# Kernel tuning notes

Measured on AMD Instinct MI355X. Metric: run time of the kernel, lower is better.

The kernel has to match this reference:

```python
import jax, jax.numpy as jnp
import numpy as np

B, H, W = 512, 36, 36
N = H * W          # 1296 oscillators
K = 8              # couplings per oscillator
EP0 = 0.1          # kura_update_rate
ANNEAL = 0.5


def setup_inputs() -> dict:
    key = jax.random.key(0)
    k = jax.random.split(key, 8)
    return {
        "input": jax.random.normal(k[0], (B, H, W), jnp.float32),
        "initial_phase": jax.random.uniform(k[1], (B, N), jnp.float32) * (2.0 * np.pi),
        "connectivity": jax.random.randint(k[2], (B, N, K), 0, N),
        "episodes": 25,
        "conv1_w": jax.random.normal(k[3], (8, 1, 3, 3), jnp.float32) * 0.1,
        "conv1_b": jnp.zeros((8,), jnp.float32),
        "conv2_w": jax.random.normal(k[4], (16, 8, 3, 3), jnp.float32) * 0.1,
        "conv2_b": jnp.zeros((16,), jnp.float32),
        "conv3_w": jax.random.normal(k[5], (32, 16, 3, 3), jnp.float32) * 0.1,
        "conv3_b": jnp.zeros((32,), jnp.float32),
        "fc_w": jax.random.normal(k[6], (108 * 8, 108 * 32), jnp.float32) * 0.02,
        "fc_b": jnp.zeros((108 * 8,), jnp.float32),
    }


def _conv3x3(x, w, b):
    y = jax.lax.conv_general_dilated(
        x, w, (1, 1), "SAME", dimension_numbers=("NCHW", "OIHW", "NCHW"))
    return y + b[None, :, None, None]


def _kuramoto(initial_phase, coupling, connectivity, steps, ep0):
    # phase: [B,N]; coupling: [B,N,K]; connectivity: [B,N,K] neighbor indices
    gather = jax.vmap(lambda p, c: p[c])  # -> [B,N,K] neighbor phases

    def step(carry, i):
        phase, ep = carry
        neigh = gather(phase, connectivity)
        # d(phase_i) = ep * sum_j coupling_ij * sin(phase_j - phase_i)
        delta = ep * (coupling * jnp.sin(neigh - phase[:, :, None])).sum(-1)
        phase = phase + delta
        ep = ep - ANNEAL * i * ep / steps  # annealed update rate
        return (phase, ep), phase

    (_, _), phases = jax.lax.scan(
        step, (initial_phase, jnp.float32(ep0)),
        jnp.arange(steps, dtype=jnp.float32))
    # record=True: trajectory includes the initial phase
    return jnp.concatenate([initial_phase[None], phases], axis=0)  # [steps+1,B,N]


def reference(input, initial_phase, connectivity, episodes,
              conv1_w, conv1_b, conv2_w, conv2_b, conv3_w, conv3_b, fc_w, fc_b):
    x = input.reshape(-1, 1, 36, 36)
    c1 = jax.nn.relu(_conv3x3(x, conv1_w, conv1_b))
    c2 = jax.nn.relu(_conv3x3(c1, conv2_w, conv2_b))
    c3 = jax.nn.sigmoid(_conv3x3(c2, conv3_w, conv3_b))
    fc = (c3.reshape(-1, 108 * 32) @ fc_w.T + fc_b).reshape(-1, N, K)  # [B,1296,8]
    phase_list = _kuramoto(initial_phase, fc, connectivity, episodes, EP0)
    return phase_list, fc
```

## Files before the change

kernel.cpp:

```cpp
#include <hip/hip_runtime.h>
#include <hip/hip_bf16.h>

#define NPOS 1296
#define BATCH 512
#define STEPS 25
#define PH_STRIDE (BATCH * NPOS)
#define PH_TOTAL ((STEPS + 1) * PH_STRIDE)
#define FC_K 3456
#define FC_N 864
#define FC_NPAD 896
#define FC_M 6144
#define KT_ITERS 54

typedef float f32x4 __attribute__((ext_vector_type(4)));
typedef __bf16 bf16x8 __attribute__((ext_vector_type(8)));

__device__ __forceinline__ ushort f2bf(float f) {
  union { float f; unsigned u; } v; v.f = f;
  unsigned r = v.u + 0x7FFFu + ((v.u >> 16) & 1u);
  return (ushort)(r >> 16);
}
__device__ __forceinline__ float bf2f(ushort h) {
  union { unsigned u; float f; } v; v.u = ((unsigned)h) << 16; return v.f;
}

__device__ __forceinline__ void async_copy16(void* lds, const void* g) {
  __builtin_amdgcn_global_load_lds(
      (const __attribute__((address_space(1))) unsigned*)g,
      (__attribute__((address_space(3))) unsigned*)lds, 16, 0, 0);
}
__device__ __forceinline__ void raw_barrier() { asm volatile("s_barrier" ::: "memory"); }
__device__ __forceinline__ void waitcnt_vm7() { asm volatile("s_waitcnt vmcnt(7)" ::: "memory"); }
__device__ __forceinline__ void waitcnt_vm0() { asm volatile("s_waitcnt vmcnt(0)" ::: "memory"); }

__global__ __launch_bounds__(256) void wprep_kernel(
    const float* __restrict__ w1, const float* __restrict__ w2, const float* __restrict__ w3,
    float* __restrict__ w1t, ushort* __restrict__ w2t, ushort* __restrict__ w3t) {
  const int tid = threadIdx.x;
  for (int i = tid; i < 72; i += 256) {
    const int s = i / 8, co = i - s * 8;
    w1t[i] = w1[co * 9 + s];
  }
  for (int i = tid; i < 16 * 96; i += 256) {
    const int co = i / 96, k = i - co * 96;
    const int s = k / 8, ci = k - s * 8;
    w2t[i] = (k < 72) ? f2bf(w2[(co * 8 + ci) * 9 + s]) : (ushort)0;
  }
  for (int i = tid; i < 32 * 160; i += 256) {
    const int co = i / 160, k = i - co * 160;
    const int s = k / 16, ci = k - s * 16;
    w3t[i] = (k < 144) ? f2bf(w3[(co * 16 + ci) * 9 + s]) : (ushort)0;
  }
}

__global__ __launch_bounds__(256, 4) void conv_fused_kernel(
    const float* __restrict__ in, const float* __restrict__ w1t, const float* __restrict__ b1,
    const ushort* __restrict__ w2t, const float* __restrict__ b2,
    const ushort* __restrict__ w3t, const float* __restrict__ b3,
    ushort* __restrict__ aout) {
  __shared__ __align__(16) float sIn[18][40];
  __shared__ __align__(16) ushort sC1[18][40][8];
  __shared__ __align__(16) ushort sC2[16][40][16];
  const int b = blockIdx.x, band = blockIdx.y, tid = threadIdx.x;
  const int r0 = band * 12;
  const int wave = tid >> 6, lane = tid & 63;
  const int quad = lane >> 4, l16 = lane & 15;
  {
    const uint4 zz = make_uint4(0, 0, 0, 0);
    for (int i = tid; i < 180; i += 256) ((uint4*)sIn)[i] = zz;
    for (int i = tid; i < 720; i += 256) ((uint4*)sC1)[i] = zz;
    for (int i = tid; i < 1280; i += 256) ((uint4*)sC2)[i] = zz;
  }
  __syncthreads();
  for (int i = tid; i < 18 * 18; i += 256) {
    const int r = i / 18, c = i - r * 18;
    const int gy = r0 - 3 + r;
    if ((unsigned)gy < 36u)
      *(float2*)&sIn[r][2 + 2 * c] = *(const float2*)(in + (size_t)b * NPOS + gy * 36 + 2 * c);
  }
  __syncthreads();
  for (int i = tid; i < 16 * 36; i += 256) {
    const int lr = i / 36, x = i - lr * 36;
    float acc[8];
#pragma unroll
    for (int co = 0; co < 8; ++co) acc[co] = b1[co];
#pragma unroll
    for (int s = 0; s < 9; ++s) {
      const int dy = s / 3, dx = s - 3 * dy;
      const float v = sIn[lr + dy][x + 1 + dx];
#pragma unroll
      for (int co = 0; co < 8; ++co) acc[co] = fmaf(w1t[s * 8 + co], v, acc[co]);
    }
    const int g1 = r0 - 2 + lr;
    if ((unsigned)g1 < 36u) {
      uint4 pk;
      pk.x = (uint)f2bf(fmaxf(acc[0], 0.f)) | ((uint)f2bf(fmaxf(acc[1], 0.f)) << 16);
      pk.y = (uint)f2bf(fmaxf(acc[2], 0.f)) | ((uint)f2bf(fmaxf(acc[3], 0.f)) << 16);
      pk.z = (uint)f2bf(fmaxf(acc[4], 0.f)) | ((uint)f2bf(fmaxf(acc[5], 0.f)) << 16);
      pk.w = (uint)f2bf(fmaxf(acc[6], 0.f)) | ((uint)f2bf(fmaxf(acc[7], 0.f)) << 16);
      *(uint4*)&sC1[lr][x + 2][0] = pk;
    }
  }
  __syncthreads();
  bf16x8 w2f[3];
#pragma unroll
  for (int f = 0; f < 3; ++f)
    w2f[f] = *(const bf16x8*)(w2t + l16 * 96 + f * 32 + quad * 8);
  const float bias2 = b2[l16];
  for (int chunk = wave; chunk < 32; chunk += 4) {
    const int m = chunk * 16 + l16;
    const int oy = m / 36, x = m - oy * 36;
    f32x4 acc = {0.f, 0.f, 0.f, 0.f};
#pragma unroll
    for (int f = 0; f < 3; ++f) {
      const int s0 = 4 * f + quad;
      const int dy = s0 / 3, dx = s0 - 3 * dy;
      const bf16x8 af = *(const bf16x8*)&sC1[oy + dy][x + 1 + dx][0];
      acc = __builtin_amdgcn_mfma_f32_16x16x32_bf16(af, w2f[f], acc, 0, 0, 0);
    }
#pragma unroll
    for (int r = 0; r < 4; ++r) {
      const int px = chunk * 16 + quad * 4 + r;
      const int oy2 = px / 36, x2 = px - oy2 * 36;
      const int g2 = r0 - 1 + oy2;
      if (px < 504 && (unsigned)g2 < 36u)
        sC2[oy2][x2 + 2][l16] = f2bf(fmaxf(acc[r] + bias2, 0.f));
    }
  }
  __syncthreads();
  bf16x8 w3f[2][5];
#pragma unroll
  for (int t = 0; t < 2; ++t)
#pragma unroll
    for (int f = 0; f < 5; ++f)
      w3f[t][f] = *(const bf16x8*)(w3t + (t * 16 + l16) * 160 + f * 32 + quad * 8);
  const float bias3a = b3[l16], bias3b = b3[16 + l16];
  ushort* ob = aout + (size_t)b * (32 * NPOS) + r0 * 36;
  for (int chunk = wave; chunk < 27; chunk += 4) {
    const int m = chunk * 16 + l16;
    const int oy = m / 36, x = m - oy * 36;
    f32x4 acc0 = {0.f, 0.f, 0.f, 0.f}, acc1 = {0.f, 0.f, 0.f, 0.f};
#pragma unroll
    for (int f = 0; f < 5; ++f) {
      const int s0 = 2 * f + (quad >> 1);
      const int dy = s0 / 3, dx = s0 - 3 * dy;
      const bf16x8 af = *(const bf16x8*)&sC2[oy + dy][x + 1 + dx][(quad & 1) * 8];
      acc0 = __builtin_amdgcn_mfma_f32_16x16x32_bf16(af, w3f[0][f], acc0, 0, 0, 0);
      acc1 = __builtin_amdgcn_mfma_f32_16x16x32_bf16(af, w3f[1][f], acc1, 0, 0, 0);
    }
    const int pxb = chunk * 16 + quad * 4;
    ushort4 pk;
#pragma unroll
    for (int r = 0; r < 4; ++r)
      ((ushort*)&pk)[r] = f2bf(1.f / (1.f + __expf(-(acc0[r] + bias3a))));
    *(ushort4*)(ob + (size_t)l16 * NPOS + pxb) = pk;
#pragma unroll
    for (int r = 0; r < 4; ++r)
      ((ushort*)&pk)[r] = f2bf(1.f / (1.f + __expf(-(acc1[r] + bias3b))));
    *(ushort4*)(ob + (size_t)(16 + l16) * NPOS + pxb) = pk;
  }
}

__global__ __launch_bounds__(256) void wcvt_kernel(const float* __restrict__ w, ushort* __restrict__ wb) {
  const int idx = blockIdx.x * 256 + threadIdx.x;
  if (idx >= FC_NPAD * FC_K) return;
  const int n = idx / FC_K;
  wb[idx] = (n < FC_N) ? f2bf(w[idx]) : (ushort)0;
}

__global__ __launch_bounds__(256) void gemm_kernel(
    const ushort* __restrict__ A, const ushort* __restrict__ Bt,
    const float* __restrict__ bias, float* __restrict__ C) {
  __shared__ __align__(16) ushort smem[2][14336];
  const int tid = threadIdx.x;
  const int lin = blockIdx.x;
  const int xcd = lin & 7, g = lin >> 3;
  const int bn = g % 7;
  const int bm = xcd + 8 * (g / 7);
  const int row0 = bm * 96, col0 = bn * 128;
  const int wave = tid >> 6, lane = tid & 63;
  const int wr = (wave >> 1) * 48, wc = (wave & 1) * 64;
  const int quad = lane >> 4, l16 = lane & 15;
  const int oswz = (quad ^ ((l16 >> 1) & 3)) * 8;
  f32x4 acc[3][4] = {};

  const int rr = lane >> 2;
  const int soct = ((lane & 3) ^ ((lane >> 3) & 3)) * 8;
  const ushort* gsrc[7];
  const ushort* ldst[7];
  {
    const int s = wave >> 1;
    if ((wave & 1) == 0) {
#pragma unroll
      for (int j = 0; j < 6; ++j) {
        gsrc[j] = A + ((size_t)row0 + j * 16 + rr) * FC_K + s * 32 + soct;
        ldst[j] = &smem[0][s * 3072 + j * 512];
      }
      gsrc[6] = Bt + ((size_t)col0 + rr) * FC_K + s * 32 + soct;
      ldst[6] = &smem[0][6144 + s * 4096];
    } else {
#pragma unroll
      for (int j = 0; j < 7; ++j) {
        gsrc[j] = Bt + ((size_t)col0 + (j + 1) * 16 + rr) * FC_K + s * 32 + soct;
        ldst[j] = &smem[0][6144 + s * 4096 + (j + 1) * 512];
      }
    }
  }
#pragma unroll
  for (int j = 0; j < 7; ++j) async_copy16((void*)ldst[j], gsrc[j]);
#pragma unroll
  for (int j = 0; j < 7; ++j) async_copy16((void*)(ldst[j] + 14336), gsrc[j] + 64);

  for (int kt = 0; kt < KT_ITERS; ++kt) {
    const int p = kt & 1;
    waitcnt_vm7();
    raw_barrier();
    const ushort* base = &smem[p][0];
#pragma unroll
    for (int s = 0; s < 2; ++s) {
      bf16x8 af[3], bfr[4];
#pragma unroll
      for (int t = 0; t < 3; ++t)
        af[t] = *(const bf16x8*)(base + s * 3072 + (wr + t * 16 + l16) * 32 + oswz);
#pragma unroll
      for (int t = 0; t < 4; ++t)
        bfr[t] = *(const bf16x8*)(base + 6144 + s * 4096 + (wc + t * 16 + l16) * 32 + oswz);
#pragma unroll
      for (int tm = 0; tm < 3; ++tm)
#pragma unroll
        for (int tn = 0; tn < 4; ++tn)
          acc[tm][tn] = __builtin_amdgcn_mfma_f32_16x16x32_bf16(af[tm], bfr[tn], acc[tm][tn], 0, 0, 0);
    }
    raw_barrier();
    int kn = kt + 2;
    if (kn >= KT_ITERS) kn -= KT_ITERS;
    const int koff = kn * 64;
#pragma unroll
    for (int j = 0; j < 7; ++j) async_copy16((void*)(ldst[j] + p * 14336), gsrc[j] + koff);
  }
  waitcnt_vm0();

#pragma unroll
  for (int tn = 0; tn < 4; ++tn) {
    const int col = col0 + wc + tn * 16 + l16;
    if (col < FC_N) {
      const float bv = bias[col];
#pragma unroll
      for (int tm = 0; tm < 3; ++tm) {
#pragma unroll
        for (int r = 0; r < 4; ++r) {
          const int row = row0 + wr + tm * 16 + quad * 4 + r;
          C[(size_t)row * FC_N + col] = acc[tm][tn][r] + bv;
        }
      }
    }
  }
}

__global__ __launch_bounds__(512) void kuramoto_kernel(
    const float* __restrict__ ph0, const int* __restrict__ conn,
    const float* __restrict__ cpl, float* __restrict__ out) {
  __shared__ float2 sc[2][NPOS];
  const int b = blockIdx.x, tid = threadIdx.x;
  int rj[3][8];
  float rc[3][8];
  float myph[3];
  float2 mysc[3];
#pragma unroll
  for (int s = 0; s < 3; ++s) {
    const int i = tid + s * 512;
    if (i < NPOS) {
      const float p = ph0[(size_t)b * NPOS + i];
      myph[s] = p;
      __builtin_nontemporal_store(p, out + (size_t)b * NPOS + i);
      float sn, cn;
      __sincosf(p, &sn, &cn);
      mysc[s] = make_float2(sn, cn);
      sc[0][i] = mysc[s];
      const size_t base = (size_t)b * (NPOS * 8) + (size_t)i * 8;
      const int4 j0 = *(const int4*)(conn + base);
      const int4 j1 = *(const int4*)(conn + base + 4);
      const float4 c0 = *(const float4*)(cpl + base);
      const float4 c1 = *(const float4*)(cpl + base + 4);
      rj[s][0] = j0.x; rj[s][1] = j0.y; rj[s][2] = j0.z; rj[s][3] = j0.w;
      rj[s][4] = j1.x; rj[s][5] = j1.y; rj[s][6] = j1.z; rj[s][7] = j1.w;
      rc[s][0] = c0.x; rc[s][1] = c0.y; rc[s][2] = c0.z; rc[s][3] = c0.w;
      rc[s][4] = c1.x; rc[s][5] = c1.y; rc[s][6] = c1.z; rc[s][7] = c1.w;
    }
  }
  float ep = 0.1f;
  for (int t = 0; t < STEPS; ++t) {
    __syncthreads();
    const int cur = t & 1;
    float* op = out + (size_t)(t + 1) * PH_STRIDE + (size_t)b * NPOS;
#pragma unroll
    for (int s = 0; s < 3; ++s) {
      const int i = tid + s * 512;
      if (i < NPOS) {
        float ss = 0.f, cc = 0.f;
#pragma unroll
        for (int k = 0; k < 8; ++k) {
          const float2 v = sc[cur][rj[s][k]];
          ss = fmaf(rc[s][k], v.x, ss);
          cc = fmaf(rc[s][k], v.y, cc);
        }
        const float np = myph[s] + ep * (mysc[s].y * ss - mysc[s].x * cc);
        myph[s] = np;
        __builtin_nontemporal_store(np, op + i);
        float sn, cn;
        __sincosf(np, &sn, &cn);
        mysc[s] = make_float2(sn, cn);
        sc[cur ^ 1][i] = mysc[s];
      }
    }
    ep = ep * (1.0f - 0.02f * (float)t);
  }
}

extern "C" void kernel_launch(void* const* d_in, const int* in_sizes, int n_in,
                              void* d_out, int out_size, void* d_ws, size_t ws_size,
                              hipStream_t stream) {
  const float* input = (const float*)d_in[0];
  const float* ph0   = (const float*)d_in[1];
  const int*   conn  = (const int*)d_in[2];
  const float* w1 = (const float*)d_in[4];
  const float* b1 = (const float*)d_in[5];
  const float* w2 = (const float*)d_in[6];
  const float* b2 = (const float*)d_in[7];
  const float* w3 = (const float*)d_in[8];
  const float* b3 = (const float*)d_in[9];
  const float* fcw = (const float*)d_in[10];
  const float* fcb = (const float*)d_in[11];
  float* out = (float*)d_out;

  ushort* Abuf = (ushort*)d_ws;
  ushort* Wbuf = (ushort*)((char*)d_ws + 42467328);
  float*  w1t  = (float*)((char*)d_ws + 48660480);
  ushort* w2t  = (ushort*)((char*)d_ws + 48660768);
  ushort* w3t  = (ushort*)((char*)d_ws + 48663840);
  float* fcout = out + PH_TOTAL;

  wprep_kernel<<<1, 256, 0, stream>>>(w1, w2, w3, w1t, w2t, w3t);
  wcvt_kernel<<<(FC_NPAD * FC_K) / 256, 256, 0, stream>>>(fcw, Wbuf);
  conv_fused_kernel<<<dim3(BATCH, 3), 256, 0, stream>>>(input, w1t, b1, w2t, b2, w3t, b3, Abuf);
  gemm_kernel<<<448, 256, 0, stream>>>(Abuf, Wbuf, fcb, fcout);
  kuramoto_kernel<<<BATCH, 512, 0, stream>>>(ph0, conn, fcout, out);
}
```

Baseline: 249.1 us.

## Fuse conv, FC GEMM and Kuramoto into one persistent megakernel with grid barriers

Replaces the five separate launches (weight prep, weight conversion, conv, GEMM, Kuramoto) with a single persistent kernel of 512 blocks. Phases are separated by atomic grid barriers, and a memset resets the barrier counters on each call. This removes launch gaps and inter-kernel drain. Small conv weights are now transposed into LDS per block, and the Kuramoto stage runs 256 threads per batch with 6 oscillators per thread instead of 512 threads. The costs are higher register pressure, a launch-bounds occupancy target of 2 blocks per CU, lower parallelism in the Kuramoto stage, and reliance on all 512 blocks being co-resident for the barriers to avoid deadlock.

```diff
diff --git a/kernel.cpp b/kernel.cpp
--- a/kernel.cpp
+++ b/kernel.cpp
@@ -9,8 +9,9 @@
 #define FC_K 3456
 #define FC_N 864
 #define FC_NPAD 896
-#define FC_M 6144
 #define KT_ITERS 54
+#define NBLK 512
+#define NTHR 256
 
 typedef float f32x4 __attribute__((ext_vector_type(4)));
 typedef __bf16 bf16x8 __attribute__((ext_vector_type(8)));
@@ -20,9 +21,6 @@
   unsigned r = v.u + 0x7FFFu + ((v.u >> 16) & 1u);
   return (ushort)(r >> 16);
 }
-__device__ __forceinline__ float bf2f(ushort h) {
-  union { unsigned u; float f; } v; v.u = ((unsigned)h) << 16; return v.f;
-}
 
 __device__ __forceinline__ void async_copy16(void* lds, const void* g) {
   __builtin_amdgcn_global_load_lds(
@@ -33,287 +31,304 @@
 __device__ __forceinline__ void waitcnt_vm7() { asm volatile("s_waitcnt vmcnt(7)" ::: "memory"); }
 __device__ __forceinline__ void waitcnt_vm0() { asm volatile("s_waitcnt vmcnt(0)" ::: "memory"); }
 
-__global__ __launch_bounds__(256) void wprep_kernel(
-    const float* __restrict__ w1, const float* __restrict__ w2, const float* __restrict__ w3,
-    float* __restrict__ w1t, ushort* __restrict__ w2t, ushort* __restrict__ w3t) {
-  const int tid = threadIdx.x;
-  for (int i = tid; i < 72; i += 256) {
-    const int s = i / 8, co = i - s * 8;
-    w1t[i] = w1[co * 9 + s];
+__device__ __forceinline__ void grid_barrier(int* bar) {
+  __threadfence();
+  __syncthreads();
+  if (threadIdx.x == 0) {
+    __hip_atomic_fetch_add(bar, 1, __ATOMIC_RELEASE, __HIP_MEMORY_SCOPE_AGENT);
+    while (__hip_atomic_load(bar, __ATOMIC_ACQUIRE, __HIP_MEMORY_SCOPE_AGENT) < NBLK)
+      __builtin_amdgcn_s_sleep(2);
   }
-  for (int i = tid; i < 16 * 96; i += 256) {
-    const int co = i / 96, k = i - co * 96;
-    const int s = k / 8, ci = k - s * 8;
-    w2t[i] = (k < 72) ? f2bf(w2[(co * 8 + ci) * 9 + s]) : (ushort)0;
-  }
-  for (int i = tid; i < 32 * 160; i += 256) {
-    const int co = i / 160, k = i - co * 160;
-    const int s = k / 16, ci = k - s * 16;
-    w3t[i] = (k < 144) ? f2bf(w3[(co * 16 + ci) * 9 + s]) : (ushort)0;
-  }
-}
-
-__global__ __launch_bounds__(256, 4) void conv_fused_kernel(
-    const float* __restrict__ in, const float* __restrict__ w1t, const float* __restrict__ b1,
-    const ushort* __restrict__ w2t, const float* __restrict__ b2,
-    const ushort* __restrict__ w3t, const float* __restrict__ b3,
-    ushort* __restrict__ aout) {
-  __shared__ __align__(16) float sIn[18][40];
-  __shared__ __align__(16) ushort sC1[18][40][8];
-  __shared__ __align__(16) ushort sC2[16][40][16];
-  const int b = blockIdx.x, band = blockIdx.y, tid = threadIdx.x;
-  const int r0 = band * 12;
+  __syncthreads();
+  __threadfence();
+}
+
+struct ConvSh {
+  float  sIn[18][40];
+  ushort sC1[18][40][8];
+  ushort sC2[16][40][16];
+  ushort w2t[16 * 96];
+  ushort w3t[32 * 160];
+};
+union ShMem {
+  ConvSh a;
+  ushort g[2][14336];
+  float2 sc[2][NPOS];
+};
+
+__global__ __launch_bounds__(NTHR, 2) void megakernel(
+    const float* __restrict__ in, const float* __restrict__ w1, const float* __restrict__ b1,
+    const float* __restrict__ w2, const float* __restrict__ b2,
+    const float* __restrict__ w3, const float* __restrict__ b3,
+    const float* __restrict__ fcw, const float* __restrict__ fcb,
+    const float* __restrict__ ph0, const int* __restrict__ conn,
+    ushort* __restrict__ Abuf, ushort* __restrict__ Wbuf,
+    int* __restrict__ bar, float* __restrict__ out) {
+  __shared__ __align__(16) ShMem sh;
+  const int tid = threadIdx.x, blk = blockIdx.x;
   const int wave = tid >> 6, lane = tid & 63;
   const int quad = lane >> 4, l16 = lane & 15;
+
   {
-    const uint4 zz = make_uint4(0, 0, 0, 0);
-    for (int i = tid; i < 180; i += 256) ((uint4*)sIn)[i] = zz;
-    for (int i = tid; i < 720; i += 256) ((uint4*)sC1)[i] = zz;
-    for (int i = tid; i < 1280; i += 256) ((uint4*)sC2)[i] = zz;
+    for (int idx = blk * NTHR + tid; idx < FC_NPAD * FC_K; idx += NBLK * NTHR) {
+      const int n = idx / FC_K;
+      Wbuf[idx] = (n < FC_N) ? f2bf(fcw[idx]) : (ushort)0;
+    }
+    for (int i = tid; i < 16 * 96; i += NTHR) {
+      const int co = i / 96, k = i - co * 96, s = k >> 3, ci = k & 7;
+      sh.a.w2t[i] = (k < 72) ? f2bf(w2[(co * 8 + ci) * 9 + s]) : (ushort)0;
+    }
+    for (int i = tid; i < 32 * 160; i += NTHR) {
+      const int co = i / 160, k = i - co * 160, s = k >> 4, ci = k & 15;
+      sh.a.w3t[i] = (k < 144) ? f2bf(w3[(co * 16 + ci) * 9 + s]) : (ushort)0;
+    }
+    __syncthreads();
+    bf16x8 w2f[3];
+#pragma unroll
+    for (int f = 0; f < 3; ++f)
+      w2f[f] = *(const bf16x8*)(sh.a.w2t + l16 * 96 + f * 32 + quad * 8);
+    bf16x8 w3f[2][5];
+#pragma unroll
+    for (int t = 0; t < 2; ++t)
+#pragma unroll
+      for (int f = 0; f < 5; ++f)
+        w3f[t][f] = *(const bf16x8*)(sh.a.w3t + (t * 16 + l16) * 160 + f * 32 + quad * 8);
+    float b1v[8];
+#pragma unroll
+    for (int co = 0; co < 8; ++co) b1v[co] = b1[co];
+    const float bias2 = b2[l16];
+    const float bias3a = b3[l16], bias3b = b3[16 + l16];
+
+    for (int task = blk; task < 3 * BATCH; task += NBLK) {
+      const int b = task & 511, band = task >> 9;
+      const int r0 = band * 12;
+      __syncthreads();
+      {
+        const uint4 zz = make_uint4(0, 0, 0, 0);
+        for (int i = tid; i < 180; i += NTHR) ((uint4*)sh.a.sIn)[i] = zz;
+        for (int i = tid; i < 720; i += NTHR) ((uint4*)sh.a.sC1)[i] = zz;
+        for (int i = tid; i < 1280; i += NTHR) ((uint4*)sh.a.sC2)[i] = zz;
+      }
+      __syncthreads();
+      for (int i = tid; i < 18 * 18; i += NTHR) {
+        const int r = i / 18, c = i - r * 18;
+        const int gy = r0 - 3 + r;
+        if ((unsigned)gy < 36u)
+          *(float2*)&sh.a.sIn[r][2 + 2 * c] = *(const float2*)(in + (size_t)b * NPOS + gy * 36 + 2 * c);
+      }
+      __syncthreads();
+      for (int i = tid; i < 16 * 36; i += NTHR) {
+        const int lr = i / 36, x = i - lr * 36;
+        float acc[8];
+#pragma unroll
+        for (int co = 0; co < 8; ++co) acc[co] = b1v[co];
+#pragma unroll
+        for (int s = 0; s < 9; ++s) {
+          const int dy = s / 3, dx = s - 3 * dy;
+          const float v = sh.a.sIn[lr + dy][x + 1 + dx];
+#pragma unroll
+          for (int co = 0; co < 8; ++co) acc[co] = fmaf(w1[co * 9 + s], v, acc[co]);
+        }
+        const int g1 = r0 - 2 + lr;
+        if ((unsigned)g1 < 36u) {
+          uint4 pk;
+          pk.x = (uint)f2bf(fmaxf(acc[0], 0.f)) | ((uint)f2bf(fmaxf(acc[1], 0.f)) << 16);
+          pk.y = (uint)f2bf(fmaxf(acc[2], 0.f)) | ((uint)f2bf(fmaxf(acc[3], 0.f)) << 16);
+          pk.z = (uint)f2bf(fmaxf(acc[4], 0.f)) | ((uint)f2bf(fmaxf(acc[5], 0.f)) << 16);
+          pk.w = (uint)f2bf(fmaxf(acc[6], 0.f)) | ((uint)f2bf(fmaxf(acc[7], 0.f)) << 16);
+          *(uint4*)&sh.a.sC1[lr][x + 2][0] = pk;
+        }
+      }
+      __syncthreads();
+      for (int chunk = wave; chunk < 32; chunk += 4) {
+        const int m = chunk * 16 + l16;
+        const int oy = m / 36, x = m - oy * 36;
+        f32x4 acc = {0.f, 0.f, 0.f, 0.f};
+#pragma unroll
+        for (int f = 0; f < 3; ++f) {
+          const int s0 = 4 * f + quad;
+          const int dy = s0 / 3, dx = s0 - 3 * dy;
+          const bf16x8 af = *(const bf16x8*)&sh.a.sC1[oy + dy][x + 1 + dx][0];
+          acc = __builtin_amdgcn_mfma_f32_16x16x32_bf16(af, w2f[f], acc, 0, 0, 0);
+        }
+#pragma unroll
+        for (int r = 0; r < 4; ++r) {
+          const int px = chunk * 16 + quad * 4 + r;
+          const int oy2 = px / 36, x2 = px - oy2 * 36;
+          const int g2 = r0 - 1 + oy2;
+          if (px < 504 && (unsigned)g2 < 36u)
+            sh.a.sC2[oy2][x2 + 2][l16] = f2bf(fmaxf(acc[r] + bias2, 0.f));
+        }
+      }
+      __syncthreads();
+      ushort* ob = Abuf + (size_t)b * (32 * NPOS) + r0 * 36;
+      for (int chunk = wave; chunk < 27; chunk += 4) {
+        const int m = chunk * 16 + l16;
+        const int oy = m / 36, x = m - oy * 36;
+        f32x4 acc0 = {0.f, 0.f, 0.f, 0.f}, acc1 = {0.f, 0.f, 0.f, 0.f};
+#pragma unroll
+        for (int f = 0; f < 5; ++f) {
+          const int s0 = 2 * f + (quad >> 1);
+          const int dy = s0 / 3, dx = s0 - 3 * dy;
+          const bf16x8 af = *(const bf16x8*)&sh.a.sC2[oy + dy][x + 1 + dx][(quad & 1) * 8];
+          acc0 = __builtin_amdgcn_mfma_f32_16x16x32_bf16(af, w3f[0][f], acc0, 0, 0, 0);
+          acc1 = __builtin_amdgcn_mfma_f32_16x16x32_bf16(af, w3f[1][f], acc1, 0, 0, 0);
+        }
+        const int pxb = chunk * 16 + quad * 4;
+        ushort4 pk;
+#pragma unroll
+        for (int r = 0; r < 4; ++r)
+          ((ushort*)&pk)[r] = f2bf(1.f / (1.f + __expf(-(acc0[r] + bias3a))));
+        *(ushort4*)(ob + (size_t)l16 * NPOS + pxb) = pk;
+#pragma unroll
+        for (int r = 0; r < 4; ++r)
+          ((ushort*)&pk)[r] = f2bf(1.f / (1.f + __expf(-(acc1[r] + bias3b))));
+        *(ushort4*)(ob + (size_t)(16 + l16) * NPOS + pxb) = pk;
+      }
+    }
   }
-  __syncthreads();
-  for (int i = tid; i < 18 * 18; i += 256) {
-    const int r = i / 18, c = i - r * 18;
-    const int gy = r0 - 3 + r;
-    if ((unsigned)gy < 36u)
-      *(float2*)&sIn[r][2 + 2 * c] = *(const float2*)(in + (size_t)b * NPOS + gy * 36 + 2 * c);
+  grid_barrier(bar + 0);
+
+  if (blk < 448) {
+    const int xcd = blk & 7, grp = blk >> 3;
+    const int bn = grp % 7;
+    const int bm = xcd + 8 * (grp / 7);
+    const int row0 = bm * 96, col0 = bn * 128;
+    const int wr = (wave >> 1) * 48, wc = (wave & 1) * 64;
+    const int oswz = (quad ^ ((l16 >> 1) & 3)) * 8;
+    f32x4 acc[3][4] = {};
+
+    const int rr = lane >> 2;
+    const int soct = ((lane & 3) ^ ((lane >> 3) & 3)) * 8;
+    const ushort* gsrc[7];
+    const ushort* ldst[7];
+    {
+      const int s = wave >> 1;
+      if ((wave & 1) == 0) {
+#pragma unroll
+        for (int j = 0; j < 6; ++j) {
+          gsrc[j] = Abuf + ((size_t)row0 + j * 16 + rr) * FC_K + s * 32 + soct;
+          ldst[j] = &sh.g[0][s * 3072 + j * 512];
+        }
+        gsrc[6] = Wbuf + ((size_t)col0 + rr) * FC_K + s * 32 + soct;
+        ldst[6] = &sh.g[0][6144 + s * 4096];
+      } else {
+#pragma unroll
+        for (int j = 0; j < 7; ++j) {
+          gsrc[j] = Wbuf + ((size_t)col0 + (j + 1) * 16 + rr) * FC_K + s * 32 + soct;
+          ldst[j] = &sh.g[0][6144 + s * 4096 + (j + 1) * 512];
+        }
+      }
+    }
+#pragma unroll
+    for (int j = 0; j < 7; ++j) async_copy16((void*)ldst[j], gsrc[j]);
+#pragma unroll
+    for (int j = 0; j < 7; ++j) async_copy16((void*)(ldst[j] + 14336), gsrc[j] + 64);
+
+    for (int kt = 0; kt < KT_ITERS; ++kt) {
+      const int p = kt & 1;
+      waitcnt_vm7();
+      raw_barrier();
+      const ushort* base = &sh.g[p][0];
+#pragma unroll
+      for (int s = 0; s < 2; ++s) {
+        bf16x8 af[3], bfr[4];
+#pragma unroll
+        for (int t = 0; t < 3; ++t)
+          af[t] = *(const bf16x8*)(base + s * 3072 + (wr + t * 16 + l16) * 32 + oswz);
+#pragma unroll
+        for (int t = 0; t < 4; ++t)
+          bfr[t] = *(const bf16x8*)(base + 6144 + s * 4096 + (wc + t * 16 + l16) * 32 + oswz);
+#pragma unroll
+        for (int tm = 0; tm < 3; ++tm)
+#pragma unroll
+          for (int tn = 0; tn < 4; ++tn)
+            acc[tm][tn] = __builtin_amdgcn_mfma_f32_16x16x32_bf16(af[tm], bfr[tn], acc[tm][tn], 0, 0, 0);
+      }
+      raw_barrier();
+      int kn = kt + 2;
+      if (kn >= KT_ITERS) kn -= KT_ITERS;
+      const int koff = kn * 64;
+#pragma unroll
+      for (int j = 0; j < 7; ++j) async_copy16((void*)(ldst[j] + p * 14336), gsrc[j] + koff);
+    }
+    waitcnt_vm0();
+
+    float* C = out + PH_TOTAL;
+#pragma unroll
+    for (int tn = 0; tn < 4; ++tn) {
+      const int col = col0 + wc + tn * 16 + l16;
+      if (col < FC_N) {
+        const float bv = fcb[col];
+#pragma unroll
+        for (int tm = 0; tm < 3; ++tm) {
+#pragma unroll
+          for (int r = 0; r < 4; ++r) {
+            const int row = row0 + wr + tm * 16 + quad * 4 + r;
+            C[(size_t)row * FC_N + col] = acc[tm][tn][r] + bv;
+          }
+        }
+      }
+    }
   }
-  __syncthreads();
-  for (int i = tid; i < 16 * 36; i += 256) {
-    const int lr = i / 36, x = i - lr * 36;
-    float acc[8];
-#pragma unroll
-    for (int co = 0; co < 8; ++co) acc[co] = b1[co];
-#pragma unroll
-    for (int s = 0; s < 9; ++s) {
-      const int dy = s / 3, dx = s - 3 * dy;
-      const float v = sIn[lr + dy][x + 1 + dx];
-#pragma unroll
-      for (int co = 0; co < 8; ++co) acc[co] = fmaf(w1t[s * 8 + co], v, acc[co]);
-    }
-    const int g1 = r0 - 2 + lr;
-    if ((unsigned)g1 < 36u) {
-      uint4 pk;
-      pk.x = (uint)f2bf(fmaxf(acc[0], 0.f)) | ((uint)f2bf(fmaxf(acc[1], 0.f)) << 16);
-      pk.y = (uint)f2bf(fmaxf(acc[2], 0.f)) | ((uint)f2bf(fmaxf(acc[3], 0.f)) << 16);
-      pk.z = (uint)f2bf(fmaxf(acc[4], 0.f)) | ((uint)f2bf(fmaxf(acc[5], 0.f)) << 16);
-      pk.w = (uint)f2bf(fmaxf(acc[6], 0.f)) | ((uint)f2bf(fmaxf(acc[7], 0.f)) << 16);
-      *(uint4*)&sC1[lr][x + 2][0] = pk;
-    }
-  }
-  __syncthreads();
-  bf16x8 w2f[3];
-#pragma unroll
-  for (int f = 0; f < 3; ++f)
-    w2f[f] = *(const bf16x8*)(w2t + l16 * 96 + f * 32 + quad * 8);
-  const float bias2 = b2[l16];
-  for (int chunk = wave; chunk < 32; chunk += 4) {
-    const int m = chunk * 16 + l16;
-    const int oy = m / 36, x = m - oy * 36;
-    f32x4 acc = {0.f, 0.f, 0.f, 0.f};
-#pragma unroll
-    for (int f = 0; f < 3; ++f) {
-      const int s0 = 4 * f + quad;
-      const int dy = s0 / 3, dx = s0 - 3 * dy;
-      const bf16x8 af = *(const bf16x8*)&sC1[oy + dy][x + 1 + dx][0];
-      acc = __builtin_amdgcn_mfma_f32_16x16x32_bf16(af, w2f[f], acc, 0, 0, 0);
-    }
-#pragma unroll
-    for (int r = 0; r < 4; ++r) {
-      const int px = chunk * 16 + quad * 4 + r;
-      const int oy2 = px / 36, x2 = px - oy2 * 36;
-      const int g2 = r0 - 1 + oy2;
-      if (px < 504 && (unsigned)g2 < 36u)
-        sC2[oy2][x2 + 2][l16] = f2bf(fmaxf(acc[r] + bias2, 0.f));
-    }
-  }
-  __syncthreads();
-  bf16x8 w3f[2][5];
-#pragma unroll
-  for (int t = 0; t < 2; ++t)
-#pragma unroll
-    for (int f = 0; f < 5; ++f)
-      w3f[t][f] = *(const bf16x8*)(w3t + (t * 16 + l16) * 160 + f * 32 + quad * 8);
-  const float bias3a = b3[l16], bias3b = b3[16 + l16];
-  ushort* ob = aout + (size_t)b * (32 * NPOS) + r0 * 36;
-  for (int chunk = wave; chunk < 27; chunk += 4) {
-    const int m = chunk * 16 + l16;
-    const int oy = m / 36, x = m - oy * 36;
-    f32x4 acc0 = {0.f, 0.f, 0.f, 0.f}, acc1 = {0.f, 0.f, 0.f, 0.f};
-#pragma unroll
-    for (int f = 0; f < 5; ++f) {
-      const int s0 = 2 * f + (quad >> 1);
-      const int dy = s0 / 3, dx = s0 - 3 * dy;
-      const bf16x8 af = *(const bf16x8*)&sC2[oy + dy][x + 1 + dx][(quad & 1) * 8];
-      acc0 = __builtin_amdgcn_mfma_f32_16x16x32_bf16(af, w3f[0][f], acc0, 0, 0, 0);
-      acc1 = __builtin_amdgcn_mfma_f32_16x16x32_bf16(af, w3f[1][f], acc1, 0, 0, 0);
-    }
-    const int pxb = chunk * 16 + quad * 4;
-    ushort4 pk;
-#pragma unroll
-    for (int r = 0; r < 4; ++r)
-      ((ushort*)&pk)[r] = f2bf(1.f / (1.f + __expf(-(acc0[r] + bias3a))));
-    *(ushort4*)(ob + (size_t)l16 * NPOS + pxb) = pk;
-#pragma unroll
-    for (int r = 0; r < 4; ++r)
-      ((ushort*)&pk)[r] = f2bf(1.f / (1.f + __expf(-(acc1[r] + bias3b))));
-    *(ushort4*)(ob + (size_t)(16 + l16) * NPOS + pxb) = pk;
-  }
-}
-
-__global__ __launch_bounds__(256) void wcvt_kernel(const float* __restrict__ w, ushort* __restrict__ wb) {
-  const int idx = blockIdx.x * 256 + threadIdx.x;
-  if (idx >= FC_NPAD * FC_K) return;
-  const int n = idx / FC_K;
-  wb[idx] = (n < FC_N) ? f2bf(w[idx]) : (ushort)0;
-}
-
-__global__ __launch_bounds__(256) void gemm_kernel(
-    const ushort* __restrict__ A, const ushort* __restrict__ Bt,
-    const float* __restrict__ bias, float* __restrict__ C) {
-  __shared__ __align__(16) ushort smem[2][14336];
-  const int tid = threadIdx.x;
-  const int lin = blockIdx.x;
-  const int xcd = lin & 7, g = lin >> 3;
-  const int bn = g % 7;
-  const int bm = xcd + 8 * (g / 7);
-  const int row0 = bm * 96, col0 = bn * 128;
-  const int wave = tid >> 6, lane = tid & 63;
-  const int wr = (wave >> 1) * 48, wc = (wave & 1) * 64;
-  const int quad = lane >> 4, l16 = lane & 15;
-  const int oswz = (quad ^ ((l16 >> 1) & 3)) * 8;
-  f32x4 acc[3][4] = {};
-
-  const int rr = lane >> 2;
-  const int soct = ((lane & 3) ^ ((lane >> 3) & 3)) * 8;
-  const ushort* gsrc[7];
-  const ushort* ldst[7];
+  grid_barrier(bar + 1);
+
   {
-    const int s = wave >> 1;
-    if ((wave & 1) == 0) {
-#pragma unroll
-      for (int j = 0; j < 6; ++j) {
-        gsrc[j] = A + ((size_t)row0 + j * 16 + rr) * FC_K + s * 32 + soct;
-        ldst[j] = &smem[0][s * 3072 + j * 512];
-      }
-      gsrc[6] = Bt + ((size_t)col0 + rr) * FC_K + s * 32 + soct;
-      ldst[6] = &smem[0][6144 + s * 4096];
-    } else {
-#pragma unroll
-      for (int j = 0; j < 7; ++j) {
-        gsrc[j] = Bt + ((size_t)col0 + (j + 1) * 16 + rr) * FC_K + s * 32 + soct;
-        ldst[j] = &smem[0][6144 + s * 4096 + (j + 1) * 512];
-      }
-    }
-  }
-#pragma unroll
-  for (int j = 0; j < 7; ++j) async_copy16((void*)ldst[j], gsrc[j]);
-#pragma unroll
-  for (int j = 0; j < 7; ++j) async_copy16((void*)(ldst[j] + 14336), gsrc[j] + 64);
-
-  for (int kt = 0; kt < KT_ITERS; ++kt) {
-    const int p = kt & 1;
-    waitcnt_vm7();
-    raw_barrier();
-    const ushort* base = &smem[p][0];
-#pragma unroll
-    for (int s = 0; s < 2; ++s) {
-      bf16x8 af[3], bfr[4];
-#pragma unroll
-      for (int t = 0; t < 3; ++t)
-        af[t] = *(const bf16x8*)(base + s * 3072 + (wr + t * 16 + l16) * 32 + oswz);
-#pragma unroll
-      for (int t = 0; t < 4; ++t)
-        bfr[t] = *(const bf16x8*)(base + 6144 + s * 4096 + (wc + t * 16 + l16) * 32 + oswz);
-#pragma unroll
-      for (int tm = 0; tm < 3; ++tm)
-#pragma unroll
-        for (int tn = 0; tn < 4; ++tn)
-          acc[tm][tn] = __builtin_amdgcn_mfma_f32_16x16x32_bf16(af[tm], bfr[tn], acc[tm][tn], 0, 0, 0);
-    }
-    raw_barrier();
-    int kn = kt + 2;
-    if (kn >= KT_ITERS) kn -= KT_ITERS;
-    const int koff = kn * 64;
-#pragma unroll
-    for (int j = 0; j < 7; ++j) async_copy16((void*)(ldst[j] + p * 14336), gsrc[j] + koff);
-  }
-  waitcnt_vm0();
-
-#pragma unroll
-  for (int tn = 0; tn < 4; ++tn) {
-    const int col = col0 + wc + tn * 16 + l16;
-    if (col < FC_N) {
-      const float bv = bias[col];
-#pragma unroll
-      for (int tm = 0; tm < 3; ++tm) {
-#pragma unroll
-        for (int r = 0; r < 4; ++r) {
-          const int row = row0 + wr + tm * 16 + quad * 4 + r;
-          C[(size_t)row * FC_N + col] = acc[tm][tn][r] + bv;
-        }
-      }
-    }
-  }
-}
-
-__global__ __launch_bounds__(512) void kuramoto_kernel(
-    const float* __restrict__ ph0, const int* __restrict__ conn,
-    const float* __restrict__ cpl, float* __restrict__ out) {
-  __shared__ float2 sc[2][NPOS];
-  const int b = blockIdx.x, tid = threadIdx.x;
-  int rj[3][8];
-  float rc[3][8];
-  float myph[3];
-  float2 mysc[3];
-#pragma unroll
-  for (int s = 0; s < 3; ++s) {
-    const int i = tid + s * 512;
-    if (i < NPOS) {
-      const float p = ph0[(size_t)b * NPOS + i];
-      myph[s] = p;
-      __builtin_nontemporal_store(p, out + (size_t)b * NPOS + i);
-      float sn, cn;
-      __sincosf(p, &sn, &cn);
-      mysc[s] = make_float2(sn, cn);
-      sc[0][i] = mysc[s];
-      const size_t base = (size_t)b * (NPOS * 8) + (size_t)i * 8;
-      const int4 j0 = *(const int4*)(conn + base);
-      const int4 j1 = *(const int4*)(conn + base + 4);
-      const float4 c0 = *(const float4*)(cpl + base);
-      const float4 c1 = *(const float4*)(cpl + base + 4);
-      rj[s][0] = j0.x; rj[s][1] = j0.y; rj[s][2] = j0.z; rj[s][3] = j0.w;
-      rj[s][4] = j1.x; rj[s][5] = j1.y; rj[s][6] = j1.z; rj[s][7] = j1.w;
-      rc[s][0] = c0.x; rc[s][1] = c0.y; rc[s][2] = c0.z; rc[s][3] = c0.w;
-      rc[s][4] = c1.x; rc[s][5] = c1.y; rc[s][6] = c1.z; rc[s][7] = c1.w;
-    }
-  }
-  float ep = 0.1f;
-  for (int t = 0; t < STEPS; ++t) {
-    __syncthreads();
-    const int cur = t & 1;
-    float* op = out + (size_t)(t + 1) * PH_STRIDE + (size_t)b * NPOS;
-#pragma unroll
-    for (int s = 0; s < 3; ++s) {
-      const int i = tid + s * 512;
+    const int b = blk;
+    const float* cpl = out + PH_TOTAL;
+    int rj[6][8];
+    float rc[6][8];
+    float myph[6];
+    float2 mysc[6];
+#pragma unroll
+    for (int s = 0; s < 6; ++s) {
+      const int i = tid + (s << 8);
       if (i < NPOS) {
-        float ss = 0.f, cc = 0.f;
-#pragma unroll
-        for (int k = 0; k < 8; ++k) {
-          const float2 v = sc[cur][rj[s][k]];
-          ss = fmaf(rc[s][k], v.x, ss);
-          cc = fmaf(rc[s][k], v.y, cc);
-        }
-        const float np = myph[s] + ep * (mysc[s].y * ss - mysc[s].x * cc);
-        myph[s] = np;
-        __builtin_nontemporal_store(np, op + i);
+        const float p = ph0[(size_t)b * NPOS + i];
+        myph[s] = p;
+        __builtin_nontemporal_store(p, out + (size_t)b * NPOS + i);
         float sn, cn;
-        __sincosf(np, &sn, &cn);
+        __sincosf(p, &sn, &cn);
         mysc[s] = make_float2(sn, cn);
-        sc[cur ^ 1][i] = mysc[s];
-      }
-    }
-    ep = ep * (1.0f - 0.02f * (float)t);
+        sh.sc[0][i] = mysc[s];
+        const size_t base = (size_t)b * (NPOS * 8) + (size_t)i * 8;
+        const int4 j0 = *(const int4*)(conn + base);
+        const int4 j1 = *(const int4*)(conn + base + 4);
+        const float4 c0 = *(const float4*)(cpl + base);
+        const float4 c1 = *(const float4*)(cpl + base + 4);
+        rj[s][0] = j0.x; rj[s][1] = j0.y; rj[s][2] = j0.z; rj[s][3] = j0.w;
+        rj[s][4] = j1.x; rj[s][5] = j1.y; rj[s][6] = j1.z; rj[s][7] = j1.w;
+        rc[s][0] = c0.x; rc[s][1] = c0.y; rc[s][2] = c0.z; rc[s][3] = c0.w;
+        rc[s][4] = c1.x; rc[s][5] = c1.y; rc[s][6] = c1.z; rc[s][7] = c1.w;
+      }
+    }
+    float ep = 0.1f;
+    for (int t = 0; t < STEPS; ++t) {
+      __syncthreads();
+      const int cur = t & 1;
+      float* op = out + (size_t)(t + 1) * PH_STRIDE + (size_t)b * NPOS;
+#pragma unroll
+      for (int s = 0; s < 6; ++s) {
+        const int i = tid + (s << 8);
+        if (i < NPOS) {
+          float ss = 0.f, cc = 0.f;
+#pragma unroll
+          for (int k = 0; k < 8; ++k) {
+            const float2 v = sh.sc[cur][rj[s][k]];
+            ss = fmaf(rc[s][k], v.x, ss);
+            cc = fmaf(rc[s][k], v.y, cc);
+          }
+          const float np = myph[s] + ep * (mysc[s].y * ss - mysc[s].x * cc);
+          myph[s] = np;
+          __builtin_nontemporal_store(np, op + i);
+          float sn, cn;
+          __sincosf(np, &sn, &cn);
+          mysc[s] = make_float2(sn, cn);
+          sh.sc[cur ^ 1][i] = mysc[s];
+        }
+      }
+      ep = ep * (1.0f - 0.02f * (float)t);
+    }
   }
 }
 
@@ -335,14 +350,9 @@
 
   ushort* Abuf = (ushort*)d_ws;
   ushort* Wbuf = (ushort*)((char*)d_ws + 42467328);
-  float*  w1t  = (float*)((char*)d_ws + 48660480);
-  ushort* w2t  = (ushort*)((char*)d_ws + 48660768);
-  ushort* w3t  = (ushort*)((char*)d_ws + 48663840);
-  float* fcout = out + PH_TOTAL;
-
-  wprep_kernel<<<1, 256, 0, stream>>>(w1, w2, w3, w1t, w2t, w3t);
-  wcvt_kernel<<<(FC_NPAD * FC_K) / 256, 256, 0, stream>>>(fcw, Wbuf);
-  conv_fused_kernel<<<dim3(BATCH, 3), 256, 0, stream>>>(input, w1t, b1, w2t, b2, w3t, b3, Abuf);
-  gemm_kernel<<<448, 256, 0, stream>>>(Abuf, Wbuf, fcb, fcout);
-  kuramoto_kernel<<<BATCH, 512, 0, stream>>>(ph0, conn, fcout, out);
-}
+  int*    bar  = (int*)((char*)d_ws + 48660480);
+
+  hipMemsetAsync((void*)bar, 0, 16, stream);
+  megakernel<<<NBLK, NTHR, 0, stream>>>(input, w1, b1, w2, b2, w3, b3, fcw, fcb,
+                                        ph0, conn, Abuf, Wbuf, bar, out);
+}
```

Result: slower. 690.4 us (+177.2%).

## Fold weight prep and FC weight conversion into conv kernel

Applied to the files above, without the earlier changes.

Removes the separate weight-prep and FC-weight bf16 conversion launches. The conv kernel now converts a slice of the FC weights per block, and each block builds its own MFMA weight fragments directly from the fp32 conv weights. This saves two kernel launches and their serialization on the stream. In exchange, every conv block does redundant strided global loads and conversions for its weight fragments, and the FC conversion traffic now competes with the conv work.

```diff
diff --git a/kernel.cpp b/kernel.cpp
--- a/kernel.cpp
+++ b/kernel.cpp
@@ -14,15 +14,13 @@
 
 typedef float f32x4 __attribute__((ext_vector_type(4)));
 typedef __bf16 bf16x8 __attribute__((ext_vector_type(8)));
+typedef ushort u16x8 __attribute__((ext_vector_type(8)));
 
 __device__ __forceinline__ ushort f2bf(float f) {
   union { float f; unsigned u; } v; v.f = f;
   unsigned r = v.u + 0x7FFFu + ((v.u >> 16) & 1u);
   return (ushort)(r >> 16);
 }
-__device__ __forceinline__ float bf2f(ushort h) {
-  union { unsigned u; float f; } v; v.u = ((unsigned)h) << 16; return v.f;
-}
 
 __device__ __forceinline__ void async_copy16(void* lds, const void* g) {
   __builtin_amdgcn_global_load_lds(
@@ -33,30 +31,11 @@
 __device__ __forceinline__ void waitcnt_vm7() { asm volatile("s_waitcnt vmcnt(7)" ::: "memory"); }
 __device__ __forceinline__ void waitcnt_vm0() { asm volatile("s_waitcnt vmcnt(0)" ::: "memory"); }
 
-__global__ __launch_bounds__(256) void wprep_kernel(
-    const float* __restrict__ w1, const float* __restrict__ w2, const float* __restrict__ w3,
-    float* __restrict__ w1t, ushort* __restrict__ w2t, ushort* __restrict__ w3t) {
-  const int tid = threadIdx.x;
-  for (int i = tid; i < 72; i += 256) {
-    const int s = i / 8, co = i - s * 8;
-    w1t[i] = w1[co * 9 + s];
-  }
-  for (int i = tid; i < 16 * 96; i += 256) {
-    const int co = i / 96, k = i - co * 96;
-    const int s = k / 8, ci = k - s * 8;
-    w2t[i] = (k < 72) ? f2bf(w2[(co * 8 + ci) * 9 + s]) : (ushort)0;
-  }
-  for (int i = tid; i < 32 * 160; i += 256) {
-    const int co = i / 160, k = i - co * 160;
-    const int s = k / 16, ci = k - s * 16;
-    w3t[i] = (k < 144) ? f2bf(w3[(co * 16 + ci) * 9 + s]) : (ushort)0;
-  }
-}
-
 __global__ __launch_bounds__(256, 4) void conv_fused_kernel(
-    const float* __restrict__ in, const float* __restrict__ w1t, const float* __restrict__ b1,
-    const ushort* __restrict__ w2t, const float* __restrict__ b2,
-    const ushort* __restrict__ w3t, const float* __restrict__ b3,
+    const float* __restrict__ in, const float* __restrict__ w1, const float* __restrict__ b1,
+    const float* __restrict__ w2, const float* __restrict__ b2,
+    const float* __restrict__ w3, const float* __restrict__ b3,
+    const float* __restrict__ fcw, ushort* __restrict__ Wbuf,
     ushort* __restrict__ aout) {
   __shared__ __align__(16) float sIn[18][40];
   __shared__ __align__(16) ushort sC1[18][40][8];
@@ -65,12 +44,47 @@
   const int r0 = band * 12;
   const int wave = tid >> 6, lane = tid & 63;
   const int quad = lane >> 4, l16 = lane & 15;
+
+  {
+    const int lb = blockIdx.y * BATCH + blockIdx.x;
+    for (int idx = lb * 256 + tid; idx < FC_NPAD * FC_K; idx += 1536 * 256) {
+      const int n = idx / FC_K;
+      Wbuf[idx] = (n < FC_N) ? f2bf(fcw[idx]) : (ushort)0;
+    }
+  }
   {
     const uint4 zz = make_uint4(0, 0, 0, 0);
     for (int i = tid; i < 180; i += 256) ((uint4*)sIn)[i] = zz;
     for (int i = tid; i < 720; i += 256) ((uint4*)sC1)[i] = zz;
     for (int i = tid; i < 1280; i += 256) ((uint4*)sC2)[i] = zz;
   }
+  bf16x8 w2f[3];
+#pragma unroll
+  for (int f = 0; f < 3; ++f) {
+    const int s = 4 * f + quad;
+    union { u16x8 u; bf16x8 bv; } cv;
+#pragma unroll
+    for (int j = 0; j < 8; ++j)
+      cv.u[j] = (s < 9) ? f2bf(w2[(l16 * 8 + j) * 9 + s]) : (ushort)0;
+    w2f[f] = cv.bv;
+  }
+  bf16x8 w3f[2][5];
+#pragma unroll
+  for (int t = 0; t < 2; ++t)
+#pragma unroll
+    for (int f = 0; f < 5; ++f) {
+      const int s = 2 * f + (quad >> 1);
+      union { u16x8 u; bf16x8 bv; } cv;
+#pragma unroll
+      for (int j = 0; j < 8; ++j)
+        cv.u[j] = (s < 9) ? f2bf(w3[((t * 16 + l16) * 16 + (quad & 1) * 8 + j) * 9 + s]) : (ushort)0;
+      w3f[t][f] = cv.bv;
+    }
+  float b1v[8];
+#pragma unroll
+  for (int co = 0; co < 8; ++co) b1v[co] = b1[co];
+  const float bias2 = b2[l16];
+  const float bias3a = b3[l16], bias3b = b3[16 + l16];
   __syncthreads();
   for (int i = tid; i < 18 * 18; i += 256) {
     const int r = i / 18, c = i - r * 18;
@@ -83,13 +97,13 @@
     const int lr = i / 36, x = i - lr * 36;
     float acc[8];
 #pragma unroll
-    for (int co = 0; co < 8; ++co) acc[co] = b1[co];
+    for (int co = 0; co < 8; ++co) acc[co] = b1v[co];
 #pragma unroll
     for (int s = 0; s < 9; ++s) {
       const int dy = s / 3, dx = s - 3 * dy;
       const float v = sIn[lr + dy][x + 1 + dx];
 #pragma unroll
-      for (int co = 0; co < 8; ++co) acc[co] = fmaf(w1t[s * 8 + co], v, acc[co]);
+      for (int co = 0; co < 8; ++co) acc[co] = fmaf(w1[co * 9 + s], v, acc[co]);
     }
     const int g1 = r0 - 2 + lr;
     if ((unsigned)g1 < 36u) {
@@ -102,11 +116,6 @@
     }
   }
   __syncthreads();
-  bf16x8 w2f[3];
-#pragma unroll
-  for (int f = 0; f < 3; ++f)
-    w2f[f] = *(const bf16x8*)(w2t + l16 * 96 + f * 32 + quad * 8);
-  const float bias2 = b2[l16];
   for (int chunk = wave; chunk < 32; chunk += 4) {
     const int m = chunk * 16 + l16;
     const int oy = m / 36, x = m - oy * 36;
@@ -128,13 +137,6 @@
     }
   }
   __syncthreads();
-  bf16x8 w3f[2][5];
-#pragma unroll
-  for (int t = 0; t < 2; ++t)
-#pragma unroll
-    for (int f = 0; f < 5; ++f)
-      w3f[t][f] = *(const bf16x8*)(w3t + (t * 16 + l16) * 160 + f * 32 + quad * 8);
-  const float bias3a = b3[l16], bias3b = b3[16 + l16];
   ushort* ob = aout + (size_t)b * (32 * NPOS) + r0 * 36;
   for (int chunk = wave; chunk < 27; chunk += 4) {
     const int m = chunk * 16 + l16;
@@ -159,13 +161,6 @@
       ((ushort*)&pk)[r] = f2bf(1.f / (1.f + __expf(-(acc1[r] + bias3b))));
     *(ushort4*)(ob + (size_t)(16 + l16) * NPOS + pxb) = pk;
   }
-}
-
-__global__ __launch_bounds__(256) void wcvt_kernel(const float* __restrict__ w, ushort* __restrict__ wb) {
-  const int idx = blockIdx.x * 256 + threadIdx.x;
-  if (idx >= FC_NPAD * FC_K) return;
-  const int n = idx / FC_K;
-  wb[idx] = (n < FC_N) ? f2bf(w[idx]) : (ushort)0;
 }
 
 __global__ __launch_bounds__(256) void gemm_kernel(
@@ -335,14 +330,10 @@
 
   ushort* Abuf = (ushort*)d_ws;
   ushort* Wbuf = (ushort*)((char*)d_ws + 42467328);
-  float*  w1t  = (float*)((char*)d_ws + 48660480);
-  ushort* w2t  = (ushort*)((char*)d_ws + 48660768);
-  ushort* w3t  = (ushort*)((char*)d_ws + 48663840);
   float* fcout = out + PH_TOTAL;
 
-  wprep_kernel<<<1, 256, 0, stream>>>(w1, w2, w3, w1t, w2t, w3t);
-  wcvt_kernel<<<(FC_NPAD * FC_K) / 256, 256, 0, stream>>>(fcw, Wbuf);
-  conv_fused_kernel<<<dim3(BATCH, 3), 256, 0, stream>>>(input, w1t, b1, w2t, b2, w3t, b3, Abuf);
+  conv_fused_kernel<<<dim3(BATCH, 3), 256, 0, stream>>>(
+      input, w1, b1, w2, b2, w3, b3, fcw, Wbuf, Abuf);
   gemm_kernel<<<448, 256, 0, stream>>>(Abuf, Wbuf, fcb, fcout);
   kuramoto_kernel<<<BATCH, 512, 0, stream>>>(ph0, conn, fcout, out);
 }
```

Result: slower. 295.2 us (+18.5%).
